# Optimization experiments

Measured on AMD Instinct MI355X. Metric: run time of the kernel, lower is better.

Reference implementation:

```python
import jax, jax.numpy as jnp
import numpy as np

BOUND = 1.0
DENSITY_SCALE = 1.0
NUM_STEPS = 128
UPSAMPLE_STEPS = 128
MAX_FAR = 5.0
MIN_NEAR = 0.2


def setup_inputs() -> dict:
    key = jax.random.key(0)
    ks = jax.random.split(key, 10)
    N, H, G = 16384, 64, 15
    return {
        "rays_o": jax.random.normal(ks[0], (N, 3), jnp.float32) * 0.5,
        "rays_d": jax.random.normal(ks[1], (N, 3), jnp.float32),
        "W1": jax.random.normal(ks[2], (3, H), jnp.float32) * 0.5,
        "b1": jnp.zeros((H,), jnp.float32),
        "W2": jax.random.normal(ks[3], (H, 1 + G), jnp.float32) * 0.3,
        "b2": jnp.zeros((1 + G,), jnp.float32),
        "Wc1": jax.random.normal(ks[4], (3 + 3 + G, H), jnp.float32) * 0.3,
        "bc1": jnp.zeros((H,), jnp.float32),
        "Wc2": jax.random.normal(ks[5], (H, 3), jnp.float32) * 0.3,
        "bc2": jnp.zeros((3,), jnp.float32),
    }


def _density(x, W1, b1, W2, b2):
    # x: [P,3] -> sigma [P], geo_feat [P,G]
    h = jax.nn.relu(x @ W1 + b1)
    o = h @ W2 + b2
    return jax.nn.softplus(o[..., 0]), o[..., 1:]


def _color(x, d, geo, Wc1, bc1, Wc2, bc2):
    inp = jnp.concatenate([x, d, geo], axis=-1)
    h = jax.nn.relu(inp @ Wc1 + bc1)
    return jax.nn.sigmoid(h @ Wc2 + bc2)


def _near_far_from_aabb(o, d, lo, hi):
    ds = jnp.where(jnp.abs(d) < 1e-8, 1e-8, d)
    t1 = (lo - o) / ds
    t2 = (hi - o) / ds
    near = jnp.max(jnp.minimum(t1, t2), axis=-1)
    far = jnp.min(jnp.maximum(t1, t2), axis=-1)
    return near, far


def _composite(z_vals, sigma, sample_dist):
    # z_vals, sigma: [N,S]; sample_dist: [N,1]
    deltas = z_vals[..., 1:] - z_vals[..., :-1]
    deltas = jnp.concatenate([deltas, sample_dist * jnp.ones_like(deltas[..., :1])], axis=-1)
    alphas = 1.0 - jnp.exp(-deltas * DENSITY_SCALE * sigma)
    shifted = jnp.concatenate([jnp.ones_like(alphas[..., :1]), 1.0 - alphas + 1e-15], axis=-1)
    weights = alphas * jnp.cumprod(shifted, axis=-1)[..., :-1]
    return weights, deltas


def _sample_pdf(bins, weights, n_samples):
    # bins: [N,M+1], weights: [N,M]  (deterministic, det=True)
    weights = weights + 1e-5
    pdf = weights / jnp.sum(weights, axis=-1, keepdims=True)
    cdf = jnp.cumsum(pdf, axis=-1)
    cdf = jnp.concatenate([jnp.zeros_like(cdf[..., :1]), cdf], axis=-1)  # [N,M+1]
    M = cdf.shape[-1] - 1
    u = jnp.linspace(0.5 / n_samples, 1.0 - 0.5 / n_samples, n_samples, dtype=cdf.dtype)
    u = jnp.broadcast_to(u, cdf.shape[:-1] + (n_samples,))
    inds = jax.vmap(lambda c, uu: jnp.searchsorted(c, uu, side="right"))(cdf, u)
    below = jnp.maximum(inds - 1, 0)
    above = jnp.minimum(inds, M)
    cdf0 = jnp.take_along_axis(cdf, below, axis=-1)
    cdf1 = jnp.take_along_axis(cdf, above, axis=-1)
    b0 = jnp.take_along_axis(bins, below, axis=-1)
    b1 = jnp.take_along_axis(bins, above, axis=-1)
    denom = cdf1 - cdf0
    denom = jnp.where(denom < 1e-5, jnp.ones_like(denom), denom)
    t = (u - cdf0) / denom
    return b0 + t * (b1 - b0)


def reference(rays_o, rays_d, W1, b1, W2, b2, Wc1, bc1, Wc2, bc2):
    N = rays_o.shape[0]
    rays_d = rays_d / jnp.linalg.norm(rays_d, axis=-1, keepdims=True)
    lo = jnp.full((3,), -BOUND, rays_o.dtype)
    hi = jnp.full((3,), BOUND, rays_o.dtype)

    nears, fars = _near_far_from_aabb(rays_o, rays_d, lo, hi)
    fars = jnp.maximum(jnp.minimum(fars, MAX_FAR), MIN_NEAR)
    nears = jnp.minimum(jnp.maximum(nears, MIN_NEAR), MAX_FAR)
    nears = nears[:, None]
    fars = fars[:, None]

    z_vals = nears + (fars - nears) * jnp.linspace(0.0, 1.0, NUM_STEPS, dtype=rays_o.dtype)[None, :]
    sample_dist = (fars - nears) / NUM_STEPS  # [N,1]

    xyzs = rays_o[:, None, :] + rays_d[:, None, :] * z_vals[..., None]
    xyzs = jnp.clip(xyzs, lo, hi)
    sigma, geo = _density(xyzs.reshape(-1, 3), W1, b1, W2, b2)
    sigma = sigma.reshape(N, NUM_STEPS)
    geo = geo.reshape(N, NUM_STEPS, -1)

    # --- importance resampling (no_grad block in torch) ---
    w_c, deltas_c = _composite(z_vals, sigma, sample_dist)
    z_mid = z_vals[..., :-1] + 0.5 * deltas_c[..., :-1]
    new_z = _sample_pdf(z_mid, w_c[:, 1:-1], UPSAMPLE_STEPS)
    new_z = jax.lax.stop_gradient(new_z)
    new_xyzs = rays_o[:, None, :] + rays_d[:, None, :] * new_z[..., None]
    new_xyzs = jax.lax.stop_gradient(jnp.clip(new_xyzs, lo, hi))
    new_sigma, new_geo = _density(new_xyzs.reshape(-1, 3), W1, b1, W2, b2)
    new_sigma = new_sigma.reshape(N, UPSAMPLE_STEPS)
    new_geo = new_geo.reshape(N, UPSAMPLE_STEPS, -1)

    # merge + sort along sample axis
    z_all = jnp.concatenate([z_vals, new_z], axis=1)
    idx = jnp.argsort(z_all, axis=1)
    z_all = jnp.take_along_axis(z_all, idx, axis=1)
    xyz_all = jnp.take_along_axis(jnp.concatenate([xyzs, new_xyzs], axis=1), idx[..., None], axis=1)
    sigma_all = jnp.take_along_axis(jnp.concatenate([sigma, new_sigma], axis=1), idx, axis=1)
    geo_all = jnp.take_along_axis(jnp.concatenate([geo, new_geo], axis=1), idx[..., None], axis=1)

    weights, _ = _composite(z_all, sigma_all, sample_dist)
    S = z_all.shape[1]
    dirs = jnp.broadcast_to(rays_d[:, None, :], (N, S, 3))
    mask = weights > 1e-4
    rgb = _color(xyz_all.reshape(-1, 3), dirs.reshape(-1, 3), geo_all.reshape(-1, geo_all.shape[-1]), Wc1, bc1, Wc2, bc2)
    rgbs = jnp.where(mask.reshape(-1)[:, None], rgb, 0.0).reshape(N, S, 3)

    weights_sum = jnp.sum(weights, axis=-1)
    image = jnp.sum(weights[..., None] * rgbs, axis=-2)
    image = image + (1.0 - weights_sum)[..., None] * 1.0  # white bg
    return image
```

## Files before the change

### kernel.cpp

```cpp
#include <hip/hip_runtime.h>
#include <hip/hip_fp16.h>
#include <math.h>

#define NRAYS 16384
#define HID 64

typedef float    float4_ __attribute__((ext_vector_type(4)));
typedef _Float16 half8   __attribute__((ext_vector_type(8)));
typedef __fp16   fp16x2  __attribute__((ext_vector_type(2)));

__device__ __forceinline__ float clip1(float v){ return fminf(fmaxf(v,-1.f),1.f); }
__device__ __forceinline__ float softplusf_(float x){
  return fmaxf(x,0.f) + __logf(1.f + __expf(-fabsf(x)));
}
__device__ __forceinline__ float sigmoidf_(float x){
  return __fdividef(1.f, 1.f + __expf(-x));
}

__device__ __forceinline__ unsigned int pkh(float a, float b){
  union { fp16x2 h; unsigned int u; } cv;
  cv.h = __builtin_amdgcn_cvt_pkrtz(a, b);
  return cv.u;
}
__device__ __forceinline__ unsigned long long pk64(float4_ a){
  return (unsigned long long)pkh(a[0],a[1]) | ((unsigned long long)pkh(a[2],a[3])<<32);
}
__device__ __forceinline__ unsigned int relu_pk(unsigned int x){
  unsigned int y;
  __asm__("v_pk_max_f16 %0, %1, 0" : "=v"(y) : "v"(x));
  return y;
}

__device__ __forceinline__ void load_ray(const float* ro, const float* rd, int r,
    float& ox,float& oy,float& oz,float& dx,float& dy,float& dz){
  ox=ro[3*r]; oy=ro[3*r+1]; oz=ro[3*r+2];
  dx=rd[3*r]; dy=rd[3*r+1]; dz=rd[3*r+2];
  float inv = 1.f/sqrtf(dx*dx+dy*dy+dz*dz);
  dx*=inv; dy*=inv; dz*=inv;
}

__device__ __forceinline__ void aabb_nf(float ox,float oy,float oz,float dx,float dy,float dz,
    float& nears,float& fars){
  float dsx = (fabsf(dx)<1e-8f)?1e-8f:dx;
  float dsy = (fabsf(dy)<1e-8f)?1e-8f:dy;
  float dsz = (fabsf(dz)<1e-8f)?1e-8f:dz;
  float t1x=(-1.f-ox)/dsx, t2x=(1.f-ox)/dsx;
  float t1y=(-1.f-oy)/dsy, t2y=(1.f-oy)/dsy;
  float t1z=(-1.f-oz)/dsz, t2z=(1.f-oz)/dsz;
  float nr = fmaxf(fmaxf(fminf(t1x,t2x),fminf(t1y,t2y)),fminf(t1z,t2z));
  float fr = fminf(fminf(fmaxf(t1x,t2x),fmaxf(t1y,t2y)),fmaxf(t1z,t2z));
  fars  = fmaxf(fminf(fr,5.f),0.2f);
  nears = fminf(fmaxf(nr,0.2f),5.f);
}

__device__ __forceinline__ float wave_excl_chunk(float chunk, int lane, float& total){
  float incl = chunk;
  #pragma unroll
  for(int off=1; off<64; off<<=1){
    float n = __shfl_up(incl, off, 64);
    if (lane >= off) incl += n;
  }
  total = __shfl(incl, 63, 64);
  return incl - chunk;
}

__global__ void prep_weights(const float* __restrict__ W1, const float* __restrict__ W2,
                             const float* __restrict__ Wc1, const float* __restrict__ Wc2,
                             unsigned short* __restrict__ wb){
  int idx = blockIdx.x*256 + threadIdx.x;
  if (idx >= 6144) return;
  int f = idx>>3, j = idx&7, lane = f&63, slot = f>>6, q = lane>>4, c = lane&15;
  int k = q*8+j;
  float v = 0.f;
  if (slot < 4){        if (k<3) v = W1[k*HID + slot*16 + c]; }
  else if (slot < 6){   int h=(slot-4)*32+k; v = W2[h*16 + c]; }
  else if (slot < 10){  int mt=slot-6;
                        int row = (k==0)? -1 : (k<16 ? 5+k : (k<22 ? k-16 : -1));
                        if (row>=0) v = Wc1[row*HID + mt*16 + c]; }
  else {                int h=(slot-10)*32+k; if (c<3) v = Wc2[h*3 + c]; }
  wb[idx] = __half_as_ushort(__float2half_rn(v));
}

__device__ __forceinline__ void storeH(unsigned short* H, float4_ a, int t, int hbase){
  unsigned int lo = relu_pk(pkh(a[0],a[1]));
  unsigned int hi = relu_pk(pkh(a[2],a[3]));
  *(unsigned long long*)&H[hbase + t*256] =
      (unsigned long long)lo | ((unsigned long long)hi<<32);
}

__global__ __launch_bounds__(128) void nerf_fused(
    const float* __restrict__ ro, const float* __restrict__ rd,
    const float* __restrict__ b1, const float* __restrict__ b2,
    const float* __restrict__ bc1, const float* __restrict__ bc2,
    const unsigned short* __restrict__ wb, float* __restrict__ out)
{
  __shared__ __align__(16) unsigned short Hfrag[2][2][1024];
  __shared__ __align__(16) unsigned short GeoAll[2][4096];
  __shared__ __align__(16) unsigned short sig16[2][256];
  __shared__ __align__(16) float zBs[2][128];
  __shared__ __align__(16) float zMc[2][264];
  __shared__ __align__(16) float wL[2][256];

  const int tid = threadIdx.x, lane = tid&63, wv = tid>>6;
  const int q = lane>>4, c = lane&15;
  const int r = blockIdx.x*2 + wv;

  float ox,oy,oz,dx,dy,dz;
  load_ray(ro,rd,r,ox,oy,oz,dx,dy,dz);
  float nears,fars; aabb_nf(ox,oy,oz,dx,dy,dz,nears,fars);
  const float step  = (fars-nears)*(1.f/127.f);
  const float sdist = (fars-nears)*(1.f/128.f);
  const bool asc = (nears <= fars);

  const half8* WF = (const half8*)wb;
  half8 aW1T[4], aW2T[2], aWc1T[4], aWc2T[2];
  #pragma unroll
  for(int t=0;t<4;t++){ aW1T[t] = WF[t*64+lane]; aWc1T[t] = WF[(6+t)*64+lane]; }
  #pragma unroll
  for(int k=0;k<2;k++){ aW2T[k] = WF[(4+k)*64+lane]; aWc2T[k] = WF[(10+k)*64+lane]; }
  float4_ b1v[4], bc1v[4];
  #pragma unroll
  for(int t=0;t<4;t++){
    b1v[t]  = *(const float4_*)&b1[t*16+q*4];
    bc1v[t] = *(const float4_*)&bc1[t*16+q*4];
  }
  const float4_ bTd = *(const float4_*)&b2[q*4];
  float4_ bTc = (float4_){0.f,0.f,0.f,0.f};
  if (q==0){ bTc[0]=bc2[0]; bTc[1]=bc2[1]; bTc[2]=bc2[2]; }

  unsigned short* H0 = &Hfrag[wv][0][0];
  unsigned short* H1 = &Hfrag[wv][1][0];
  unsigned short* Geo = &GeoAll[wv][0];
  unsigned short* sgw = sig16[wv];
  float* zBsw = zBs[wv];
  float* cdfw = zMc[wv];
  float* zMw  = zMc[wv];
  float* wLw  = wL[wv];
  const int hbase = (q>>1)*128 + c*8 + (q&1)*4;
  const int lread = lane*8;

  #pragma unroll
  for(int p=0;p<4;p++){
    const int sidx0 = p*32 + c, sidx1 = p*32 + 16 + c;
    half8 bf0 = (half8)(_Float16)0, bf1 = (half8)(_Float16)0;
    if (q==0){
      float z0 = fmaf(step,(float)sidx0,nears);
      float z1 = fmaf(step,(float)sidx1,nears);
      unsigned int* u0p = (unsigned int*)&bf0;
      u0p[0] = pkh(clip1(fmaf(dx,z0,ox)), clip1(fmaf(dy,z0,oy)));
      u0p[1] = pkh(clip1(fmaf(dz,z0,oz)), 0.f);
      unsigned int* u1p = (unsigned int*)&bf1;
      u1p[0] = pkh(clip1(fmaf(dx,z1,ox)), clip1(fmaf(dy,z1,oy)));
      u1p[1] = pkh(clip1(fmaf(dz,z1,oz)), 0.f);
    }
    #pragma unroll
    for(int t=0;t<4;t++){
      float4_ a0 = __builtin_amdgcn_mfma_f32_16x16x32_f16(aW1T[t], bf0, b1v[t], 0,0,0);
      float4_ a1 = __builtin_amdgcn_mfma_f32_16x16x32_f16(aW1T[t], bf1, b1v[t], 0,0,0);
      storeH(H0, a0, t, hbase);
      storeH(H1, a1, t, hbase);
    }
    half8 h00 = *(const half8*)&H0[lread];
    half8 h01 = *(const half8*)&H0[512 + lread];
    half8 h10 = *(const half8*)&H1[lread];
    half8 h11 = *(const half8*)&H1[512 + lread];
    float4_ o0 = __builtin_amdgcn_mfma_f32_16x16x32_f16(aW2T[0], h00, bTd, 0,0,0);
    o0 = __builtin_amdgcn_mfma_f32_16x16x32_f16(aW2T[1], h01, o0, 0,0,0);
    float4_ o1 = __builtin_amdgcn_mfma_f32_16x16x32_f16(aW2T[0], h10, bTd, 0,0,0);
    o1 = __builtin_amdgcn_mfma_f32_16x16x32_f16(aW2T[1], h11, o1, 0,0,0);
    *(unsigned long long*)&Geo[sidx0*16 + q*4] = pk64(o0);
    *(unsigned long long*)&Geo[sidx1*16 + q*4] = pk64(o1);
    if (q==0){
      sgw[sidx0] = __half_as_ushort(__float2half_rn(softplusf_(o0[0])));
      sgw[sidx1] = __half_as_ushort(__float2half_rn(softplusf_(o1[0])));
    }
  }

  {
    union { unsigned int u; __half2 h; } sp;
    sp.u = *(const unsigned int*)&sgw[2*lane];
    float s0 = __half2float(__low2half(sp.h));
    float s1 = __half2float(__high2half(sp.h));
    float d0 = (2*lane   < 127) ? step*s0 : 0.f;
    float d1 = (2*lane+1 < 127) ? step*s1 : 0.f;
    float tot;
    float e0 = wave_excl_chunk(d0+d1, lane, tot);
    float w0 = (1.f-__expf(-d0))*__expf(-e0);
    float w1 = (1.f-__expf(-d1))*__expf(-(e0+d0));
    float ww0 = (lane>=1 && 2*lane<127) ? w0+1e-5f : 0.f;
    float ww1 = (2*lane+1 < 127) ? w1+1e-5f : 0.f;
    float wsum;
    float ce0 = wave_excl_chunk(ww0+ww1, lane, wsum);
    float inv = __fdividef(1.f, wsum);
    cdfw[2*lane]   = (ce0+ww0)*inv;
    cdfw[2*lane+1] = (ce0+ww0+ww1)*inv;
  }

  {
    const float u0c = 0.5f/128.f;
    const float du = (1.f - 1.f/128.f)/127.f;
    #pragma unroll
    for(int j=0;j<2;j++){
      int k = lane + j*64;
      float u = fmaf(du,(float)k,u0c);
      int lo=0, hi=127;
      while(lo<hi){ int m=(lo+hi)>>1; if (cdfw[m] <= u) lo=m+1; else hi=m; }
      int below = max(lo-1,0), above = min(lo,126);
      float c0 = cdfw[below], c1 = cdfw[above];
      float bb0 = nears + step*((float)below + 0.5f);
      float bb1 = nears + step*((float)above + 0.5f);
      float den = c1 - c0; if (den < 1e-5f) den = 1.f;
      float zf = bb0 + (u - c0)/den*(bb1 - bb0);
      zBsw[asc ? k : 127-k] = zf;
    }
  }

  #pragma unroll
  for(int p=0;p<4;p++){
    const int sidx0 = p*32 + c, sidx1 = p*32 + 16 + c;
    half8 bf0 = (half8)(_Float16)0, bf1 = (half8)(_Float16)0;
    if (q==0){
      float z0 = zBsw[sidx0];
      float z1 = zBsw[sidx1];
      unsigned int* u0p = (unsigned int*)&bf0;
      u0p[0] = pkh(clip1(fmaf(dx,z0,ox)), clip1(fmaf(dy,z0,oy)));
      u0p[1] = pkh(clip1(fmaf(dz,z0,oz)), 0.f);
      unsigned int* u1p = (unsigned int*)&bf1;
      u1p[0] = pkh(clip1(fmaf(dx,z1,ox)), clip1(fmaf(dy,z1,oy)));
      u1p[1] = pkh(clip1(fmaf(dz,z1,oz)), 0.f);
    }
    #pragma unroll
    for(int t=0;t<4;t++){
      float4_ a0 = __builtin_amdgcn_mfma_f32_16x16x32_f16(aW1T[t], bf0, b1v[t], 0,0,0);
      float4_ a1 = __builtin_amdgcn_mfma_f32_16x16x32_f16(aW1T[t], bf1, b1v[t], 0,0,0);
      storeH(H0, a0, t, hbase);
      storeH(H1, a1, t, hbase);
    }
    half8 h00 = *(const half8*)&H0[lread];
    half8 h01 = *(const half8*)&H0[512 + lread];
    half8 h10 = *(const half8*)&H1[lread];
    half8 h11 = *(const half8*)&H1[512 + lread];
    float4_ o0 = __builtin_amdgcn_mfma_f32_16x16x32_f16(aW2T[0], h00, bTd, 0,0,0);
    o0 = __builtin_amdgcn_mfma_f32_16x16x32_f16(aW2T[1], h01, o0, 0,0,0);
    float4_ o1 = __builtin_amdgcn_mfma_f32_16x16x32_f16(aW2T[0], h10, bTd, 0,0,0);
    o1 = __builtin_amdgcn_mfma_f32_16x16x32_f16(aW2T[1], h11, o1, 0,0,0);
    *(unsigned long long*)&Geo[(128+sidx0)*16 + q*4] = pk64(o0);
    *(unsigned long long*)&Geo[(128+sidx1)*16 + q*4] = pk64(o1);
    if (q==0){
      sgw[128+sidx0] = __half_as_ushort(__float2half_rn(softplusf_(o0[0])));
      sgw[128+sidx1] = __half_as_ushort(__float2half_rn(softplusf_(o1[0])));
    }
  }

  #pragma unroll
  for(int j=0;j<2;j++){
    int sA = lane + j*64;
    int i = asc ? sA : 127-sA;
    float myz = fmaf(step,(float)i,nears);
    int lo=0, hi=128;
    while(lo<hi){ int m=(lo+hi)>>1; if (zBsw[m] < myz) lo=m+1; else hi=m; }
    int pos = sA + lo;
    zMw[pos] = __uint_as_float((__float_as_uint(myz) & ~255u) | (unsigned)i);
  }
  #pragma unroll
  for(int j=0;j<2;j++){
    int k = lane + j*64;
    float myz = zBsw[k];
    int lo=0, hi=128;
    while(lo<hi){
      int m=(lo+hi)>>1;
      float Am = fmaf(step,(float)(asc?m:127-m),nears);
      if (Am <= myz) lo=m+1; else hi=m;
    }
    int pos = k + lo;
    zMw[pos] = __uint_as_float((__float_as_uint(myz) & ~255u) | (unsigned)(128+k));
  }

  {
    float4_ z4 = *(const float4_*)&zMw[4*lane];
    float z5 = zMw[4*lane+4];
    float sg0 = __half2float(*(const __half*)&sgw[__float_as_uint(z4[0]) & 255u]);
    float sg1 = __half2float(*(const __half*)&sgw[__float_as_uint(z4[1]) & 255u]);
    float sg2 = __half2float(*(const __half*)&sgw[__float_as_uint(z4[2]) & 255u]);
    float sg3 = __half2float(*(const __half*)&sgw[__float_as_uint(z4[3]) & 255u]);
    float d0 = (z4[1]-z4[0])*sg0;
    float d1 = (z4[2]-z4[1])*sg1;
    float d2 = (z4[3]-z4[2])*sg2;
    float dl = (lane==63) ? sdist : (z5 - z4[3]);
    float d3 = dl*sg3;
    float tot;
    float S = wave_excl_chunk(d0+d1+d2+d3, lane, tot);
    float4_ w4;
    w4[0] = (1.f-__expf(-d0))*__expf(-S); S += d0;
    w4[1] = (1.f-__expf(-d1))*__expf(-S); S += d1;
    w4[2] = (1.f-__expf(-d2))*__expf(-S); S += d2;
    w4[3] = (1.f-__expf(-d3))*__expf(-S);
    *(float4_*)&wLw[4*lane] = w4;
  }

  float accR=0.f, accG=0.f, accB=0.f, accW=0.f;
  #pragma unroll
  for(int p=0;p<8;p++){
    const int sidx0 = p*32 + c, sidx1 = p*32 + 16 + c;
    float g0w = wLw[sidx0];
    float g1w = wLw[sidx1];
    if (q==0){ accW += g0w + g1w; }
    unsigned long long vis = __ballot((g0w > 1e-4f) || (g1w > 1e-4f));
    if (vis == 0ull) continue;

    float z0 = zMw[sidx0], z1 = zMw[sidx1];
    int o0i = (int)(__float_as_uint(z0) & 255u);
    int o1i = (int)(__float_as_uint(z1) & 255u);
    float x0 = clip1(fmaf(dx,z0,ox)), y0 = clip1(fmaf(dy,z0,oy)), w0 = clip1(fmaf(dz,z0,oz));
    float x1 = clip1(fmaf(dx,z1,ox)), y1 = clip1(fmaf(dy,z1,oy)), w1 = clip1(fmaf(dz,z1,oz));
    half8 bcf0 = (half8)(_Float16)0, bcf1 = (half8)(_Float16)0;
    if (q < 2){
      bcf0 = *(const half8*)&Geo[o0i*16 + q*8];
      bcf1 = *(const half8*)&Geo[o1i*16 + q*8];
    } else if (q == 2){
      unsigned int* u0p = (unsigned int*)&bcf0;
      u0p[0] = pkh(x0,y0); u0p[1] = pkh(w0,dx); u0p[2] = pkh(dy,dz); u0p[3] = 0u;
      unsigned int* u1p = (unsigned int*)&bcf1;
      u1p[0] = pkh(x1,y1); u1p[1] = pkh(w1,dx); u1p[2] = pkh(dy,dz); u1p[3] = 0u;
    }
    #pragma unroll
    for(int t=0;t<4;t++){
      float4_ a0 = __builtin_amdgcn_mfma_f32_16x16x32_f16(aWc1T[t], bcf0, bc1v[t], 0,0,0);
      float4_ a1 = __builtin_amdgcn_mfma_f32_16x16x32_f16(aWc1T[t], bcf1, bc1v[t], 0,0,0);
      storeH(H0, a0, t, hbase);
      storeH(H1, a1, t, hbase);
    }
    half8 h00 = *(const half8*)&H0[lread];
    half8 h01 = *(const half8*)&H0[512 + lread];
    half8 h10 = *(const half8*)&H1[lread];
    half8 h11 = *(const half8*)&H1[512 + lread];
    float4_ oc0 = __builtin_amdgcn_mfma_f32_16x16x32_f16(aWc2T[0], h00, bTc, 0,0,0);
    oc0 = __builtin_amdgcn_mfma_f32_16x16x32_f16(aWc2T[1], h01, oc0, 0,0,0);
    float4_ oc1 = __builtin_amdgcn_mfma_f32_16x16x32_f16(aWc2T[0], h10, bTc, 0,0,0);
    oc1 = __builtin_amdgcn_mfma_f32_16x16x32_f16(aWc2T[1], h11, oc1, 0,0,0);
    if (q==0){
      if (g0w > 1e-4f){
        accR = fmaf(g0w, sigmoidf_(oc0[0]), accR);
        accG = fmaf(g0w, sigmoidf_(oc0[1]), accG);
        accB = fmaf(g0w, sigmoidf_(oc0[2]), accB);
      }
      if (g1w > 1e-4f){
        accR = fmaf(g1w, sigmoidf_(oc1[0]), accR);
        accG = fmaf(g1w, sigmoidf_(oc1[1]), accG);
        accB = fmaf(g1w, sigmoidf_(oc1[2]), accB);
      }
    }
  }

  #pragma unroll
  for(int off=32; off; off>>=1){
    accR += __shfl_down(accR, off, 64);
    accG += __shfl_down(accG, off, 64);
    accB += __shfl_down(accB, off, 64);
    accW += __shfl_down(accW, off, 64);
  }
  if (lane == 0){
    float bg = 1.f - accW;
    out[r*3+0] = accR + bg;
    out[r*3+1] = accG + bg;
    out[r*3+2] = accB + bg;
  }
}

extern "C" void kernel_launch(void* const* d_in, const int* in_sizes, int n_in,
                              void* d_out, int out_size, void* d_ws, size_t ws_size,
                              hipStream_t stream) {
  const float* ro  = (const float*)d_in[0];
  const float* rd  = (const float*)d_in[1];
  const float* W1  = (const float*)d_in[2];
  const float* b1  = (const float*)d_in[3];
  const float* W2  = (const float*)d_in[4];
  const float* b2  = (const float*)d_in[5];
  const float* Wc1 = (const float*)d_in[6];
  const float* bc1 = (const float*)d_in[7];
  const float* Wc2 = (const float*)d_in[8];
  const float* bc2 = (const float*)d_in[9];
  float* out = (float*)d_out;

  unsigned short* wb = (unsigned short*)d_ws;

  prep_weights<<<dim3(24), dim3(256), 0, stream>>>(W1, W2, Wc1, Wc2, wb);
  nerf_fused<<<dim3(NRAYS/2), dim3(128), 0, stream>>>(
      ro, rd, b1, b2, bc1, bc2, wb, out);
}
```

Measured before the change: 201.6 us.

## Fuse color MLP into density passes and drop geo feature staging

Runs the color MLP right after the density MLP for every coarse and fine sample, storing packed fp16 RGB plus sigma per sample instead of the 16-wide geo features. The compositing step then gathers precomputed colors by sorted index, so the separate post-sort color loop, the geo buffer and the weight buffer go away. In exchange, color is now computed for all 256 samples, including those the old weight-threshold ballot would have skipped. Shared memory per block shrinks considerably, which may raise occupancy.

```diff
diff --git a/kernel.cpp b/kernel.cpp
--- a/kernel.cpp
+++ b/kernel.cpp
@@ -15,6 +15,9 @@
 }
 __device__ __forceinline__ float sigmoidf_(float x){
   return __fdividef(1.f, 1.f + __expf(-x));
+}
+__device__ __forceinline__ float h2f(unsigned short u){
+  union { unsigned short s; __fp16 h; } cv; cv.s = u; return (float)cv.h;
 }
 
 __device__ __forceinline__ unsigned int pkh(float a, float b){
@@ -95,11 +98,9 @@
     const unsigned short* __restrict__ wb, float* __restrict__ out)
 {
   __shared__ __align__(16) unsigned short Hfrag[2][2][1024];
-  __shared__ __align__(16) unsigned short GeoAll[2][4096];
-  __shared__ __align__(16) unsigned short sig16[2][256];
+  __shared__ __align__(16) unsigned long long RGBS[2][256];
   __shared__ __align__(16) float zBs[2][128];
-  __shared__ __align__(16) float zMc[2][264];
-  __shared__ __align__(16) float wL[2][256];
+  __shared__ __align__(16) float zMc[2][260];
 
   const int tid = threadIdx.x, lane = tid&63, wv = tid>>6;
   const int q = lane>>4, c = lane&15;
@@ -111,6 +112,7 @@
   const float step  = (fars-nears)*(1.f/127.f);
   const float sdist = (fars-nears)*(1.f/128.f);
   const bool asc = (nears <= fars);
+  const unsigned int pk_dydz = pkh(dy,dz);
 
   const half8* WF = (const half8*)wb;
   half8 aW1T[4], aW2T[2], aWc1T[4], aWc2T[2];
@@ -130,28 +132,33 @@
 
   unsigned short* H0 = &Hfrag[wv][0][0];
   unsigned short* H1 = &Hfrag[wv][1][0];
-  unsigned short* Geo = &GeoAll[wv][0];
-  unsigned short* sgw = sig16[wv];
+  unsigned long long* RGBSw = RGBS[wv];
   float* zBsw = zBs[wv];
   float* cdfw = zMc[wv];
   float* zMw  = zMc[wv];
-  float* wLw  = wL[wv];
-  const int hbase = (q>>1)*128 + c*8 + (q&1)*4;
-  const int lread = lane*8;
-
-  #pragma unroll
-  for(int p=0;p<4;p++){
+  const int hbase  = (q>>1)*128 + c*8 + (q&1)*4;
+  const int lread  = lane*8;
+  const int gstage = c*16 + q*4;
+  const int gread  = c*16 + q*8;
+
+  auto pairbody = [&](int p, int sbase, bool coarse){
     const int sidx0 = p*32 + c, sidx1 = p*32 + 16 + c;
     half8 bf0 = (half8)(_Float16)0, bf1 = (half8)(_Float16)0;
-    if (q==0){
-      float z0 = fmaf(step,(float)sidx0,nears);
-      float z1 = fmaf(step,(float)sidx1,nears);
-      unsigned int* u0p = (unsigned int*)&bf0;
-      u0p[0] = pkh(clip1(fmaf(dx,z0,ox)), clip1(fmaf(dy,z0,oy)));
-      u0p[1] = pkh(clip1(fmaf(dz,z0,oz)), 0.f);
-      unsigned int* u1p = (unsigned int*)&bf1;
-      u1p[0] = pkh(clip1(fmaf(dx,z1,ox)), clip1(fmaf(dy,z1,oy)));
-      u1p[1] = pkh(clip1(fmaf(dz,z1,oz)), 0.f);
+    unsigned int c0a=0u,c0b=0u,c1a=0u,c1b=0u;
+    if ((q&1)==0){
+      float z0 = coarse ? fmaf(step,(float)sidx0,nears) : zBsw[sidx0];
+      float z1 = coarse ? fmaf(step,(float)sidx1,nears) : zBsw[sidx1];
+      float x0 = clip1(fmaf(dx,z0,ox)), y0 = clip1(fmaf(dy,z0,oy)), g0 = clip1(fmaf(dz,z0,oz));
+      float x1 = clip1(fmaf(dx,z1,ox)), y1 = clip1(fmaf(dy,z1,oy)), g1 = clip1(fmaf(dz,z1,oz));
+      if (q==0){
+        unsigned int* u0p = (unsigned int*)&bf0;
+        u0p[0] = pkh(x0,y0); u0p[1] = pkh(g0,0.f);
+        unsigned int* u1p = (unsigned int*)&bf1;
+        u1p[0] = pkh(x1,y1); u1p[1] = pkh(g1,0.f);
+      } else {
+        c0a = pkh(x0,y0); c0b = pkh(g0,dx);
+        c1a = pkh(x1,y1); c1b = pkh(g1,dx);
+      }
     }
     #pragma unroll
     for(int t=0;t<4;t++){
@@ -168,19 +175,49 @@
     o0 = __builtin_amdgcn_mfma_f32_16x16x32_f16(aW2T[1], h01, o0, 0,0,0);
     float4_ o1 = __builtin_amdgcn_mfma_f32_16x16x32_f16(aW2T[0], h10, bTd, 0,0,0);
     o1 = __builtin_amdgcn_mfma_f32_16x16x32_f16(aW2T[1], h11, o1, 0,0,0);
-    *(unsigned long long*)&Geo[sidx0*16 + q*4] = pk64(o0);
-    *(unsigned long long*)&Geo[sidx1*16 + q*4] = pk64(o1);
+    float sp0 = softplusf_(o0[0]);
+    float sp1 = softplusf_(o1[0]);
+    *(unsigned long long*)&H0[gstage] = pk64(o0);
+    *(unsigned long long*)&H1[gstage] = pk64(o1);
+    half8 bcf0 = (half8)(_Float16)0, bcf1 = (half8)(_Float16)0;
+    if (q < 2){
+      bcf0 = *(const half8*)&H0[gread];
+      bcf1 = *(const half8*)&H1[gread];
+    } else if (q == 2){
+      unsigned int* u0p = (unsigned int*)&bcf0;
+      u0p[0] = c0a; u0p[1] = c0b; u0p[2] = pk_dydz; u0p[3] = 0u;
+      unsigned int* u1p = (unsigned int*)&bcf1;
+      u1p[0] = c1a; u1p[1] = c1b; u1p[2] = pk_dydz; u1p[3] = 0u;
+    }
+    #pragma unroll
+    for(int t=0;t<4;t++){
+      float4_ a0 = __builtin_amdgcn_mfma_f32_16x16x32_f16(aWc1T[t], bcf0, bc1v[t], 0,0,0);
+      float4_ a1 = __builtin_amdgcn_mfma_f32_16x16x32_f16(aWc1T[t], bcf1, bc1v[t], 0,0,0);
+      storeH(H0, a0, t, hbase);
+      storeH(H1, a1, t, hbase);
+    }
+    h00 = *(const half8*)&H0[lread];
+    h01 = *(const half8*)&H0[512 + lread];
+    h10 = *(const half8*)&H1[lread];
+    h11 = *(const half8*)&H1[512 + lread];
+    float4_ oc0 = __builtin_amdgcn_mfma_f32_16x16x32_f16(aWc2T[0], h00, bTc, 0,0,0);
+    oc0 = __builtin_amdgcn_mfma_f32_16x16x32_f16(aWc2T[1], h01, oc0, 0,0,0);
+    float4_ oc1 = __builtin_amdgcn_mfma_f32_16x16x32_f16(aWc2T[0], h10, bTc, 0,0,0);
+    oc1 = __builtin_amdgcn_mfma_f32_16x16x32_f16(aWc2T[1], h11, oc1, 0,0,0);
     if (q==0){
-      sgw[sidx0] = __half_as_ushort(__float2half_rn(softplusf_(o0[0])));
-      sgw[sidx1] = __half_as_ushort(__float2half_rn(softplusf_(o1[0])));
-    }
-  }
+      RGBSw[sbase+sidx0] = pk64((float4_){sigmoidf_(oc0[0]), sigmoidf_(oc0[1]),
+                                          sigmoidf_(oc0[2]), sp0});
+      RGBSw[sbase+sidx1] = pk64((float4_){sigmoidf_(oc1[0]), sigmoidf_(oc1[1]),
+                                          sigmoidf_(oc1[2]), sp1});
+    }
+  };
+
+  #pragma unroll
+  for(int p=0;p<4;p++) pairbody(p, 0, true);
 
   {
-    union { unsigned int u; __half2 h; } sp;
-    sp.u = *(const unsigned int*)&sgw[2*lane];
-    float s0 = __half2float(__low2half(sp.h));
-    float s1 = __half2float(__high2half(sp.h));
+    float s0 = h2f(((const unsigned short*)&RGBSw[2*lane  ])[3]);
+    float s1 = h2f(((const unsigned short*)&RGBSw[2*lane+1])[3]);
     float d0 = (2*lane   < 127) ? step*s0 : 0.f;
     float d1 = (2*lane+1 < 127) ? step*s1 : 0.f;
     float tot;
@@ -216,41 +253,7 @@
   }
 
   #pragma unroll
-  for(int p=0;p<4;p++){
-    const int sidx0 = p*32 + c, sidx1 = p*32 + 16 + c;
-    half8 bf0 = (half8)(_Float16)0, bf1 = (half8)(_Float16)0;
-    if (q==0){
-      float z0 = zBsw[sidx0];
-      float z1 = zBsw[sidx1];
-      unsigned int* u0p = (unsigned int*)&bf0;
-      u0p[0] = pkh(clip1(fmaf(dx,z0,ox)), clip1(fmaf(dy,z0,oy)));
-      u0p[1] = pkh(clip1(fmaf(dz,z0,oz)), 0.f);
-      unsigned int* u1p = (unsigned int*)&bf1;
-      u1p[0] = pkh(clip1(fmaf(dx,z1,ox)), clip1(fmaf(dy,z1,oy)));
-      u1p[1] = pkh(clip1(fmaf(dz,z1,oz)), 0.f);
-    }
-    #pragma unroll
-    for(int t=0;t<4;t++){
-      float4_ a0 = __builtin_amdgcn_mfma_f32_16x16x32_f16(aW1T[t], bf0, b1v[t], 0,0,0);
-      float4_ a1 = __builtin_amdgcn_mfma_f32_16x16x32_f16(aW1T[t], bf1, b1v[t], 0,0,0);
-      storeH(H0, a0, t, hbase);
-      storeH(H1, a1, t, hbase);
-    }
-    half8 h00 = *(const half8*)&H0[lread];
-    half8 h01 = *(const half8*)&H0[512 + lread];
-    half8 h10 = *(const half8*)&H1[lread];
-    half8 h11 = *(const half8*)&H1[512 + lread];
-    float4_ o0 = __builtin_amdgcn_mfma_f32_16x16x32_f16(aW2T[0], h00, bTd, 0,0,0);
-    o0 = __builtin_amdgcn_mfma_f32_16x16x32_f16(aW2T[1], h01, o0, 0,0,0);
-    float4_ o1 = __builtin_amdgcn_mfma_f32_16x16x32_f16(aW2T[0], h10, bTd, 0,0,0);
-    o1 = __builtin_amdgcn_mfma_f32_16x16x32_f16(aW2T[1], h11, o1, 0,0,0);
-    *(unsigned long long*)&Geo[(128+sidx0)*16 + q*4] = pk64(o0);
-    *(unsigned long long*)&Geo[(128+sidx1)*16 + q*4] = pk64(o1);
-    if (q==0){
-      sgw[128+sidx0] = __half_as_ushort(__float2half_rn(softplusf_(o0[0])));
-      sgw[128+sidx1] = __half_as_ushort(__float2half_rn(softplusf_(o1[0])));
-    }
-  }
+  for(int p=0;p<4;p++) pairbody(p, 128, false);
 
   #pragma unroll
   for(int j=0;j<2;j++){
@@ -276,13 +279,22 @@
     zMw[pos] = __uint_as_float((__float_as_uint(myz) & ~255u) | (unsigned)(128+k));
   }
 
+  float accR=0.f, accG=0.f, accB=0.f, accW=0.f;
   {
     float4_ z4 = *(const float4_*)&zMw[4*lane];
     float z5 = zMw[4*lane+4];
-    float sg0 = __half2float(*(const __half*)&sgw[__float_as_uint(z4[0]) & 255u]);
-    float sg1 = __half2float(*(const __half*)&sgw[__float_as_uint(z4[1]) & 255u]);
-    float sg2 = __half2float(*(const __half*)&sgw[__float_as_uint(z4[2]) & 255u]);
-    float sg3 = __half2float(*(const __half*)&sgw[__float_as_uint(z4[3]) & 255u]);
+    int oi0 = (int)(__float_as_uint(z4[0]) & 255u);
+    int oi1 = (int)(__float_as_uint(z4[1]) & 255u);
+    int oi2 = (int)(__float_as_uint(z4[2]) & 255u);
+    int oi3 = (int)(__float_as_uint(z4[3]) & 255u);
+    unsigned long long p0 = RGBSw[oi0];
+    unsigned long long p1 = RGBSw[oi1];
+    unsigned long long p2 = RGBSw[oi2];
+    unsigned long long p3 = RGBSw[oi3];
+    float sg0 = h2f((unsigned short)(p0>>48));
+    float sg1 = h2f((unsigned short)(p1>>48));
+    float sg2 = h2f((unsigned short)(p2>>48));
+    float sg3 = h2f((unsigned short)(p3>>48));
     float d0 = (z4[1]-z4[0])*sg0;
     float d1 = (z4[2]-z4[1])*sg1;
     float d2 = (z4[3]-z4[2])*sg2;
@@ -295,60 +307,26 @@
     w4[1] = (1.f-__expf(-d1))*__expf(-S); S += d1;
     w4[2] = (1.f-__expf(-d2))*__expf(-S); S += d2;
     w4[3] = (1.f-__expf(-d3))*__expf(-S);
-    *(float4_*)&wLw[4*lane] = w4;
-  }
-
-  float accR=0.f, accG=0.f, accB=0.f, accW=0.f;
-  #pragma unroll
-  for(int p=0;p<8;p++){
-    const int sidx0 = p*32 + c, sidx1 = p*32 + 16 + c;
-    float g0w = wLw[sidx0];
-    float g1w = wLw[sidx1];
-    if (q==0){ accW += g0w + g1w; }
-    unsigned long long vis = __ballot((g0w > 1e-4f) || (g1w > 1e-4f));
-    if (vis == 0ull) continue;
-
-    float z0 = zMw[sidx0], z1 = zMw[sidx1];
-    int o0i = (int)(__float_as_uint(z0) & 255u);
-    int o1i = (int)(__float_as_uint(z1) & 255u);
-    float x0 = clip1(fmaf(dx,z0,ox)), y0 = clip1(fmaf(dy,z0,oy)), w0 = clip1(fmaf(dz,z0,oz));
-    float x1 = clip1(fmaf(dx,z1,ox)), y1 = clip1(fmaf(dy,z1,oy)), w1 = clip1(fmaf(dz,z1,oz));
-    half8 bcf0 = (half8)(_Float16)0, bcf1 = (half8)(_Float16)0;
-    if (q < 2){
-      bcf0 = *(const half8*)&Geo[o0i*16 + q*8];
-      bcf1 = *(const half8*)&Geo[o1i*16 + q*8];
-    } else if (q == 2){
-      unsigned int* u0p = (unsigned int*)&bcf0;
-      u0p[0] = pkh(x0,y0); u0p[1] = pkh(w0,dx); u0p[2] = pkh(dy,dz); u0p[3] = 0u;
-      unsigned int* u1p = (unsigned int*)&bcf1;
-      u1p[0] = pkh(x1,y1); u1p[1] = pkh(w1,dx); u1p[2] = pkh(dy,dz); u1p[3] = 0u;
-    }
-    #pragma unroll
-    for(int t=0;t<4;t++){
-      float4_ a0 = __builtin_amdgcn_mfma_f32_16x16x32_f16(aWc1T[t], bcf0, bc1v[t], 0,0,0);
-      float4_ a1 = __builtin_amdgcn_mfma_f32_16x16x32_f16(aWc1T[t], bcf1, bc1v[t], 0,0,0);
-      storeH(H0, a0, t, hbase);
-      storeH(H1, a1, t, hbase);
-    }
-    half8 h00 = *(const half8*)&H0[lread];
-    half8 h01 = *(const half8*)&H0[512 + lread];
-    half8 h10 = *(const half8*)&H1[lread];
-    half8 h11 = *(const half8*)&H1[512 + lread];
-    float4_ oc0 = __builtin_amdgcn_mfma_f32_16x16x32_f16(aWc2T[0], h00, bTc, 0,0,0);
-    oc0 = __builtin_amdgcn_mfma_f32_16x16x32_f16(aWc2T[1], h01, oc0, 0,0,0);
-    float4_ oc1 = __builtin_amdgcn_mfma_f32_16x16x32_f16(aWc2T[0], h10, bTc, 0,0,0);
-    oc1 = __builtin_amdgcn_mfma_f32_16x16x32_f16(aWc2T[1], h11, oc1, 0,0,0);
-    if (q==0){
-      if (g0w > 1e-4f){
-        accR = fmaf(g0w, sigmoidf_(oc0[0]), accR);
-        accG = fmaf(g0w, sigmoidf_(oc0[1]), accG);
-        accB = fmaf(g0w, sigmoidf_(oc0[2]), accB);
-      }
-      if (g1w > 1e-4f){
-        accR = fmaf(g1w, sigmoidf_(oc1[0]), accR);
-        accG = fmaf(g1w, sigmoidf_(oc1[1]), accG);
-        accB = fmaf(g1w, sigmoidf_(oc1[2]), accB);
-      }
+    accW = w4[0]+w4[1]+w4[2]+w4[3];
+    if (w4[0] > 1e-4f){
+      accR = fmaf(w4[0], h2f((unsigned short) p0      ), accR);
+      accG = fmaf(w4[0], h2f((unsigned short)(p0>>16) ), accG);
+      accB = fmaf(w4[0], h2f((unsigned short)(p0>>32) ), accB);
+    }
+    if (w4[1] > 1e-4f){
+      accR = fmaf(w4[1], h2f((unsigned short) p1      ), accR);
+      accG = fmaf(w4[1], h2f((unsigned short)(p1>>16) ), accG);
+      accB = fmaf(w4[1], h2f((unsigned short)(p1>>32) ), accB);
+    }
+    if (w4[2] > 1e-4f){
+      accR = fmaf(w4[2], h2f((unsigned short) p2      ), accR);
+      accG = fmaf(w4[2], h2f((unsigned short)(p2>>16) ), accG);
+      accB = fmaf(w4[2], h2f((unsigned short)(p2>>32) ), accB);
+    }
+    if (w4[3] > 1e-4f){
+      accR = fmaf(w4[3], h2f((unsigned short) p3      ), accR);
+      accG = fmaf(w4[3], h2f((unsigned short)(p3>>16) ), accG);
+      accB = fmaf(w4[3], h2f((unsigned short)(p3>>32) ), accB);
     }
   }
 
```

After: 185.1 us. -8.2%, faster.
